# Optimization experiments

Measured on AMD Instinct MI355X. Metric: run time of the kernel, lower is better.

## Reference

```python
import jax, jax.numpy as jnp
import numpy as np

N, DEG, F, H, OUT = 50000, 16, 128, 128, 64


def _lstm_aggr(neigh, w_ih, w_hh, b_ih, b_hh):
    # neigh: [N, D, F] fixed-degree neighbor features; run LSTM over D steps,
    # return final hidden state [N, H] (PyG SAGEConv 'lstm' aggregation).
    n, d, f = neigh.shape
    h_dim = w_hh.shape[1]

    def step(carry, xt):
        h, c = carry
        gates = xt @ w_ih.T + b_ih + h @ w_hh.T + b_hh  # [N, 4H]
        i, fg, g, o = jnp.split(gates, 4, axis=-1)      # torch gate order i,f,g,o
        i = jax.nn.sigmoid(i)
        fg = jax.nn.sigmoid(fg)
        g = jnp.tanh(g)
        o = jax.nn.sigmoid(o)
        c = fg * c + i * g
        h = o * jnp.tanh(c)
        return (h, c), None

    h0 = jnp.zeros((n, h_dim), neigh.dtype)
    (h, _), _ = jax.lax.scan(step, (h0, h0), jnp.swapaxes(neigh, 0, 1))
    return h


def _sage_lstm(x, src, w_ih, w_hh, b_ih, b_hh, wl, bl, wr):
    # SAGEConv: out = lin_l(lstm_aggr(x[neighbors])) + lin_r(x)
    neigh = x[src]                                   # [N, D, F] gather
    aggr = _lstm_aggr(neigh, w_ih, w_hh, b_ih, b_hh)  # [N, H]
    return aggr @ wl.T + bl + x @ wr.T


def setup_inputs() -> dict:
    key = jax.random.key(0)
    ks = jax.random.split(key, 16)
    x = jax.random.normal(ks[0], (N, F), dtype=jnp.float32)
    # fixed-degree graph: dst = arange(N) each repeated DEG times (sorted, as
    # PyG lstm aggregation requires), src random -> edge_index [2, N*DEG]
    src = jax.random.randint(ks[1], (N * DEG,), 0, N, dtype=jnp.int64)
    dst = jnp.repeat(jnp.arange(N, dtype=jnp.int64), DEG)
    edge_index = jnp.stack([src, dst])
    s = 1.0 / np.sqrt(H)
    def u(k, shape):
        return jax.random.uniform(k, shape, jnp.float32, -s, s)
    params = {
        # layer 1 (input F -> hidden H)
        "w_ih1": u(ks[2], (4 * H, F)), "w_hh1": u(ks[3], (4 * H, H)),
        "b_ih1": u(ks[4], (4 * H,)), "b_hh1": u(ks[5], (4 * H,)),
        "lin_l1_w": u(ks[6], (H, H)), "lin_l1_b": u(ks[6], (H,)),
        "lin_r1_w": u(ks[7], (H, F)),
        # layer 2 (H -> H)
        "w_ih2": u(ks[8], (4 * H, H)), "w_hh2": u(ks[9], (4 * H, H)),
        "b_ih2": u(ks[10], (4 * H,)), "b_hh2": u(ks[11], (4 * H,)),
        "lin_l2_w": u(ks[12], (H, H)), "lin_l2_b": u(ks[12], (H,)),
        "lin_r2_w": u(ks[13], (H, H)),
        # output head
        "lin_w": u(ks[14], (OUT, H)), "lin_b": u(ks[15], (OUT,)),
    }
    return {"x": x, "edge_index": edge_index, **params}


def reference(x, edge_index,
              w_ih1, w_hh1, b_ih1, b_hh1, lin_l1_w, lin_l1_b, lin_r1_w,
              w_ih2, w_hh2, b_ih2, b_hh2, lin_l2_w, lin_l2_b, lin_r2_w,
              lin_w, lin_b):
    n = x.shape[0]
    deg = edge_index.shape[1] // n
    src = edge_index[0].reshape(n, deg)  # fixed-degree neighbor matrix
    h = _sage_lstm(x, src, w_ih1, w_hh1, b_ih1, b_hh1, lin_l1_w, lin_l1_b, lin_r1_w)
    h = jax.nn.relu(h)
    h = _sage_lstm(h, src, w_ih2, w_hh2, b_ih2, b_hh2, lin_l2_w, lin_l2_b, lin_r2_w)
    h = jax.nn.relu(h)
    return h @ lin_w.T + lin_b
```

## Files before the change

kernel.cpp:

```cpp
#include <hip/hip_runtime.h>
#include <stdint.h>

#define NN 50000
#define DEG 16
#define MT 32
#define NBLK ((NN + MT - 1) / MT)
#define LOG2E 1.4426950408889634f

typedef short bf16x8 __attribute__((ext_vector_type(8)));
typedef float f32x4 __attribute__((ext_vector_type(4)));
typedef unsigned short u16;
typedef unsigned int u32;

static __device__ __forceinline__ u16 f2bf(float f) {
  union { float f; u32 u; } v; v.f = f;
  u32 u = v.u + 0x7FFFu + ((v.u >> 16) & 1u);
  return (u16)(u >> 16);
}
static __device__ __forceinline__ u32 cvtpk(float lo, float hi) {
  u32 r;
  asm("v_cvt_pk_bf16_f32 %0, %1, %2" : "=v"(r) : "v"(lo), "v"(hi));
  return r;
}
static __device__ __forceinline__ float rcp_(float x) {
  return __builtin_amdgcn_rcpf(x);
}
static __device__ __forceinline__ float ex2_(float x) {
  return __builtin_amdgcn_exp2f(x);
}
static __device__ __forceinline__ void gload_lds16(const void* g, void* l) {
  __builtin_amdgcn_global_load_lds(
      (const __attribute__((address_space(1))) void*)g,
      (__attribute__((address_space(3))) void*)l, 16, 0, 0);
}

__global__ void k_prep(const float* __restrict__ x, u16* __restrict__ xb,
                       const float* __restrict__ wih1, const float* __restrict__ whh1, u16* __restrict__ wpk1,
                       const float* __restrict__ wih2, const float* __restrict__ whh2, u16* __restrict__ wpk2,
                       const float* __restrict__ lr1, const float* __restrict__ ll1, u16* __restrict__ epk1,
                       const float* __restrict__ lr2, const float* __restrict__ ll2, u16* __restrict__ epk2,
                       const float* __restrict__ linw, u16* __restrict__ hpk,
                       const float* __restrict__ bi1, const float* __restrict__ bh1, float* __restrict__ bs1,
                       const float* __restrict__ bi2, const float* __restrict__ bh2, float* __restrict__ bs2) {
  int b = blockIdx.x;
  if (b < 128) {
    const float* wih = (b < 64) ? wih1 : wih2;
    const float* whh = (b < 64) ? whh1 : whh2;
    u16* wpk = (b < 64) ? wpk1 : wpk2;
    int t = (b & 63) * 256 + threadIdx.x;
    int lane = t & 63, kt = (t >> 6) & 7, g = (t >> 9) & 3, w = (t >> 11) & 7;
    int col = g * 128 + w * 16 + (lane & 15);
    int k0 = kt * 32 + (lane >> 4) * 8;
    float sc = (g == 2) ? 2.f * LOG2E : LOG2E;
#pragma unroll
    for (int j = 0; j < 8; ++j) {
      int k = k0 + j;
      float v = (k < 128) ? wih[col * 128 + k] : whh[col * 128 + k - 128];
      wpk[t * 8 + j] = f2bf(sc * v);
    }
  } else if (b < 160) {
    const float* lrw = (b < 144) ? lr1 : lr2;
    const float* llw = (b < 144) ? ll1 : ll2;
    u16* epk = (b < 144) ? epk1 : epk2;
    int t = ((b - 128) & 15) * 256 + threadIdx.x;
    int lane = t & 63, kt = (t >> 6) & 7, w = (t >> 9) & 7;
    int col = w * 16 + (lane & 15);
    int k0 = kt * 32 + (lane >> 4) * 8;
#pragma unroll
    for (int j = 0; j < 8; ++j) {
      int k = k0 + j;
      epk[t * 8 + j] = f2bf(k < 128 ? lrw[col * 128 + k] : llw[col * 128 + k - 128]);
    }
  } else if (b < 164) {
    int t = (b - 160) * 256 + threadIdx.x;
    int lane = t & 63, kt = (t >> 6) & 3, w = (t >> 8) & 3;
    int col = w * 16 + (lane & 15);
    int k0 = kt * 32 + (lane >> 4) * 8;
#pragma unroll
    for (int j = 0; j < 8; ++j) hpk[t * 8 + j] = f2bf(linw[col * 128 + k0 + j]);
  } else if (b < 168) {
    int t = (b - 164) * 256 + threadIdx.x;
    if (t < 1024) {
      int i = t & 511;
      float sc = ((i >> 7) == 2) ? 2.f * LOG2E : LOG2E;
      if (t < 512) bs1[i] = sc * (bi1[i] + bh1[i]);
      else bs2[i] = sc * (bi2[i] + bh2[i]);
    }
  } else {
    int i = (b - 168) * 256 + threadIdx.x;
    int stride = (gridDim.x - 168) * 256;
    for (; i < NN * 128 / 4; i += stride) {
      float4 v = ((const float4*)x)[i];
      ushort4 o;
      o.x = f2bf(v.x); o.y = f2bf(v.y); o.z = f2bf(v.z); o.w = f2bf(v.w);
      ((ushort4*)xb)[i] = o;
    }
  }
}


#define GATHER(DCODE, PDST)                                                   \
  do {                                                                        \
    int idx_;                                                                 \
    if ((DCODE) < DEG) idx_ = IDX[grow * DEG + (DCODE)];                      \
    else idx_ = (node0 + grow < NN) ? node0 + grow : NN - 1;                  \
    const char* gsw_ = (const char*)(xin + (size_t)idx_ * 128) +              \
                       ((lr * 16) ^ ((grow & 15) << 4));                      \
    gload_lds16(gsw_, (PDST) + (w * 4) * 128);                                \
  } while (0)

#define CBAR(N)                                                               \
  do {                                                                        \
    asm volatile("s_waitcnt vmcnt(" #N ") lgkmcnt(0)" ::: "memory");          \
    __builtin_amdgcn_s_barrier();                                             \
    __builtin_amdgcn_sched_barrier(0);                                        \
  } while (0)

template <int L2>
__global__ __launch_bounds__(512, 2) void k_layer(
    const u16* __restrict__ xin, const int* __restrict__ src,
    const u16* __restrict__ wpk, const float* __restrict__ bsum,
    const u16* __restrict__ epk, const float* __restrict__ linlb,
    u16* __restrict__ hout, const u16* __restrict__ hpk,
    const float* __restrict__ linb, float* __restrict__ dout) {
  __shared__ __align__(16) u16 AX[3][MT * 128];
  __shared__ __align__(16) u16 AH[2][MT * 128];
  __shared__ int IDX[MT * DEG];

  const int tid = threadIdx.x;
  const int w = tid >> 6, l = tid & 63;
  const int lr = l & 15, lh = l >> 4;
  const int node0 = blockIdx.x * MT;
  const int grow = w * 4 + lh;

  bf16x8 wreg[4][8];
#pragma unroll
  for (int g = 0; g < 4; ++g)
#pragma unroll
    for (int kt = 0; kt < 8; ++kt)
      wreg[g][kt] = *(const bf16x8*)(wpk + (size_t)(((w * 4 + g) * 8 + kt) * 64 + l) * 8);

  IDX[tid] = (node0 + (tid >> 4) < NN) ? src[node0 * DEG + tid] : 0;

  float gb[4];
#pragma unroll
  for (int g = 0; g < 4; ++g) gb[g] = bsum[g * 128 + w * 16 + lr];
  float eb = linlb[w * 16 + lr];
  __syncthreads();

  GATHER(0, AX[0]);
  GATHER(1, AX[1]);

  f32x4 c[2];
  c[0] = (f32x4){0.f, 0.f, 0.f, 0.f};
  c[1] = (f32x4){0.f, 0.f, 0.f, 0.f};
  CBAR(1);

  u16 *pA = AX[0], *pB = AX[1], *pC = AX[2];

#pragma unroll 1
  for (int step = 0; step < DEG; ++step) {
    const int cb = step & 1, nb = cb ^ 1;

    if (step < DEG - 1) GATHER(step + 2, pC);

    f32x4 acc[2][4];
#pragma unroll
    for (int mt = 0; mt < 2; ++mt)
#pragma unroll
      for (int g = 0; g < 4; ++g)
        acc[mt][g] = (f32x4){gb[g], gb[g], gb[g], gb[g]};

    __builtin_amdgcn_s_setprio(1);
#pragma unroll
    for (int kt = 0; kt < 4; ++kt) {
      bf16x8 af[2];
#pragma unroll
      for (int mt = 0; mt < 2; ++mt) {
        int row = mt * 16 + lr;
        af[mt] = *(const bf16x8*)((const char*)pA + row * 256 +
                                  ((kt * 64 + lh * 16) ^ ((row & 15) << 4)));
      }
#pragma unroll
      for (int g = 0; g < 4; ++g)
#pragma unroll
        for (int mt = 0; mt < 2; ++mt)
          acc[mt][g] = __builtin_amdgcn_mfma_f32_16x16x32_bf16(af[mt], wreg[g][kt], acc[mt][g], 0, 0, 0);
    }

    if (step) {
#pragma unroll
      for (int kt = 0; kt < 4; ++kt) {
        bf16x8 af[2];
#pragma unroll
        for (int mt = 0; mt < 2; ++mt) {
          int row = mt * 16 + lr;
          af[mt] = *(const bf16x8*)((const char*)AH[cb] + row * 256 +
                                    ((kt * 64 + lh * 16) ^ ((row & 15) << 4)));
        }
#pragma unroll
        for (int g = 0; g < 4; ++g)
#pragma unroll
          for (int mt = 0; mt < 2; ++mt)
            acc[mt][g] = __builtin_amdgcn_mfma_f32_16x16x32_bf16(af[mt], wreg[g][4 + kt], acc[mt][g], 0, 0, 0);
      }
    }
    __builtin_amdgcn_s_setprio(0);

#pragma unroll
    for (int mt = 0; mt < 2; ++mt) {
      float hv[4];
#pragma unroll
      for (int r = 0; r < 4; ++r) {
        float iv = rcp_(1.f + ex2_(-acc[mt][0][r]));
        float fv = rcp_(1.f + ex2_(-acc[mt][1][r]));
        float gv = 1.f - 2.f * rcp_(1.f + ex2_(acc[mt][2][r]));
        float ov = rcp_(1.f + ex2_(-acc[mt][3][r]));
        float cv = fv * c[mt][r] + iv * gv;
        c[mt][r] = cv;
        float th = 1.f - 2.f * rcp_(1.f + ex2_(2.f * LOG2E * cv));
        hv[r] = ov * th;
      }
      u32 pk01 = cvtpk(hv[0], hv[1]);
      u32 pk23 = cvtpk(hv[2], hv[3]);
      const int jj = 2 * (w * 16 + lr);
#pragma unroll
      for (int r = 0; r < 4; ++r) {
        int row = mt * 16 + lh * 4 + r;
        u16 hb16 = (r == 0) ? (u16)pk01 : (r == 1) ? (u16)(pk01 >> 16)
                   : (r == 2) ? (u16)pk23 : (u16)(pk23 >> 16);
        *(u16*)((char*)AH[nb] + row * 256 + (jj ^ ((row & 15) << 4))) = hb16;
      }
    }

    if (step < DEG - 1) CBAR(1);
    else CBAR(0);

    u16* t_ = pA; pA = pB; pB = t_;
    t_ = pB; pB = pC; pC = t_;
  }

  f32x4 eacc[2];
  eacc[0] = (f32x4){eb, eb, eb, eb};
  eacc[1] = (f32x4){eb, eb, eb, eb};
#pragma unroll
  for (int kt = 0; kt < 8; ++kt) {
    const u16* srcb = (kt < 4) ? pA : AH[0];
    int kb = (kt & 3) * 64 + lh * 16;
    bf16x8 af[2];
#pragma unroll
    for (int mt = 0; mt < 2; ++mt) {
      int row = mt * 16 + lr;
      af[mt] = *(const bf16x8*)((const char*)srcb + row * 256 +
                                (kb ^ ((row & 15) << 4)));
    }
    bf16x8 bf = *(const bf16x8*)(epk + (size_t)((w * 8 + kt) * 64 + l) * 8);
#pragma unroll
    for (int mt = 0; mt < 2; ++mt)
      eacc[mt] = __builtin_amdgcn_mfma_f32_16x16x32_bf16(af[mt], bf, eacc[mt], 0, 0, 0);
  }

  if constexpr (!L2) {
#pragma unroll
    for (int mt = 0; mt < 2; ++mt) {
      u32 pk01 = cvtpk(fmaxf(eacc[mt][0], 0.f), fmaxf(eacc[mt][1], 0.f));
      u32 pk23 = cvtpk(fmaxf(eacc[mt][2], 0.f), fmaxf(eacc[mt][3], 0.f));
#pragma unroll
      for (int r = 0; r < 4; ++r) {
        int node = node0 + mt * 16 + lh * 4 + r;
        if (node < NN) {
          u16 hb16 = (r == 0) ? (u16)pk01 : (r == 1) ? (u16)(pk01 >> 16)
                     : (r == 2) ? (u16)pk23 : (u16)(pk23 >> 16);
          hout[(size_t)node * 128 + w * 16 + lr] = hb16;
        }
      }
    }
  } else {
#pragma unroll
    for (int mt = 0; mt < 2; ++mt) {
      u32 pk01 = cvtpk(fmaxf(eacc[mt][0], 0.f), fmaxf(eacc[mt][1], 0.f));
      u32 pk23 = cvtpk(fmaxf(eacc[mt][2], 0.f), fmaxf(eacc[mt][3], 0.f));
      const int jj = 2 * (w * 16 + lr);
#pragma unroll
      for (int r = 0; r < 4; ++r) {
        int row = mt * 16 + lh * 4 + r;
        u16 hb16 = (r == 0) ? (u16)pk01 : (r == 1) ? (u16)(pk01 >> 16)
                   : (r == 2) ? (u16)pk23 : (u16)(pk23 >> 16);
        *(u16*)((char*)AH[1] + row * 256 + (jj ^ ((row & 15) << 4))) = hb16;
      }
    }
    __syncthreads();
    if (w < 4) {
      float hb = linb[w * 16 + lr];
      f32x4 hacc[2];
      hacc[0] = (f32x4){hb, hb, hb, hb};
      hacc[1] = (f32x4){hb, hb, hb, hb};
#pragma unroll
      for (int kt = 0; kt < 4; ++kt) {
        bf16x8 af[2];
#pragma unroll
        for (int mt = 0; mt < 2; ++mt) {
          int row = mt * 16 + lr;
          af[mt] = *(const bf16x8*)((const char*)AH[1] + row * 256 +
                                    ((kt * 64 + lh * 16) ^ ((row & 15) << 4)));
        }
        bf16x8 bf = *(const bf16x8*)(hpk + (size_t)((w * 4 + kt) * 64 + l) * 8);
#pragma unroll
        for (int mt = 0; mt < 2; ++mt)
          hacc[mt] = __builtin_amdgcn_mfma_f32_16x16x32_bf16(af[mt], bf, hacc[mt], 0, 0, 0);
      }
#pragma unroll
      for (int mt = 0; mt < 2; ++mt)
#pragma unroll
        for (int r = 0; r < 4; ++r) {
          int node = node0 + mt * 16 + lh * 4 + r;
          if (node < NN) dout[(size_t)node * 64 + w * 16 + lr] = hacc[mt][r];
        }
    }
  }
}

extern "C" void kernel_launch(void* const* d_in, const int* in_sizes, int n_in,
                              void* d_out, int out_size, void* d_ws, size_t ws_size,
                              hipStream_t stream) {
  const float* x    = (const float*)d_in[0];
  const int*   edge = (const int*)d_in[1];
  const float* wih1 = (const float*)d_in[2];
  const float* whh1 = (const float*)d_in[3];
  const float* bih1 = (const float*)d_in[4];
  const float* bhh1 = (const float*)d_in[5];
  const float* ll1w = (const float*)d_in[6];
  const float* ll1b = (const float*)d_in[7];
  const float* lr1w = (const float*)d_in[8];
  const float* wih2 = (const float*)d_in[9];
  const float* whh2 = (const float*)d_in[10];
  const float* bih2 = (const float*)d_in[11];
  const float* bhh2 = (const float*)d_in[12];
  const float* ll2w = (const float*)d_in[13];
  const float* ll2b = (const float*)d_in[14];
  const float* lr2w = (const float*)d_in[15];
  const float* linw = (const float*)d_in[16];
  const float* linb = (const float*)d_in[17];

  char* ws = (char*)d_ws;
  u16* xb    = (u16*)(ws);
  u16* h1b   = (u16*)(ws + 12800000);
  u16* wpk1  = (u16*)(ws + 25600000);
  u16* wpk2  = (u16*)(ws + 25862144);
  u16* epk1  = (u16*)(ws + 26124288);
  u16* epk2  = (u16*)(ws + 26189824);
  u16* hpk   = (u16*)(ws + 26255360);
  float* bs1 = (float*)(ws + 26271744);
  float* bs2 = (float*)(ws + 26273792);

  k_prep<<<1000, 256, 0, stream>>>(x, xb,
                                   wih1, whh1, wpk1, wih2, whh2, wpk2,
                                   lr1w, ll1w, epk1, lr2w, ll2w, epk2,
                                   linw, hpk,
                                   bih1, bhh1, bs1, bih2, bhh2, bs2);
  k_layer<0><<<NBLK, 512, 0, stream>>>(xb, edge, wpk1, bs1, epk1, ll1b,
                                       h1b, nullptr, nullptr, nullptr);
  k_layer<1><<<NBLK, 512, 0, stream>>>(h1b, edge, wpk2, bs2, epk2, ll2b,
                                       nullptr, hpk, linb, (float*)d_out);
}
```

Measured before the change: 497.9 us.

## Software-pipeline the LSTM input projection one step ahead with a 4-deep gather ring

The input-to-gate MFMA work (x_t · W_ih) for the next time step now runs before the end-of-step barrier, right after the elementwise gate update. After the barrier, only the recurrent h · W_hh part sits on the critical path of each step. To keep data ready, the neighbor-gather ring grows from 3 to 4 LDS buffers and prefetches three steps ahead. The cost is more LDS per block and accumulator registers held live across the barrier, which could add register pressure under the 512-thread, 2-block launch bounds.

```diff
diff --git a/kernel.cpp b/kernel.cpp
--- a/kernel.cpp
+++ b/kernel.cpp
@@ -116,6 +116,26 @@
     __builtin_amdgcn_sched_barrier(0);                                        \
   } while (0)
 
+#define XPART(P)                                                              \
+  do {                                                                        \
+    _Pragma("unroll") for (int mt = 0; mt < 2; ++mt)                          \
+        _Pragma("unroll") for (int g = 0; g < 4; ++g)                         \
+            acc[mt][g] = (f32x4){gb[g], gb[g], gb[g], gb[g]};                 \
+    __builtin_amdgcn_s_setprio(1);                                            \
+    _Pragma("unroll") for (int kt = 0; kt < 4; ++kt) {                        \
+      bf16x8 af[2];                                                           \
+      _Pragma("unroll") for (int mt = 0; mt < 2; ++mt) {                      \
+        int row = mt * 16 + lr;                                               \
+        af[mt] = *(const bf16x8*)((const char*)(P) + row * 256 +              \
+                                  ((kt * 64 + lh * 16) ^ ((row & 15) << 4))); \
+      }                                                                       \
+      _Pragma("unroll") for (int g = 0; g < 4; ++g)                           \
+          _Pragma("unroll") for (int mt = 0; mt < 2; ++mt)                    \
+              acc[mt][g] = __builtin_amdgcn_mfma_f32_16x16x32_bf16(af[mt], wreg[g][kt], acc[mt][g], 0, 0, 0); \
+    }                                                                         \
+    __builtin_amdgcn_s_setprio(0);                                            \
+  } while (0)
+
 template <int L2>
 __global__ __launch_bounds__(512, 2) void k_layer(
     const u16* __restrict__ xin, const int* __restrict__ src,
@@ -123,7 +143,7 @@
     const u16* __restrict__ epk, const float* __restrict__ linlb,
     u16* __restrict__ hout, const u16* __restrict__ hpk,
     const float* __restrict__ linb, float* __restrict__ dout) {
-  __shared__ __align__(16) u16 AX[3][MT * 128];
+  __shared__ __align__(16) u16 AX[4][MT * 128];
   __shared__ __align__(16) u16 AH[2][MT * 128];
   __shared__ int IDX[MT * DEG];
 
@@ -150,45 +170,27 @@
 
   GATHER(0, AX[0]);
   GATHER(1, AX[1]);
+  GATHER(2, AX[2]);
 
   f32x4 c[2];
   c[0] = (f32x4){0.f, 0.f, 0.f, 0.f};
   c[1] = (f32x4){0.f, 0.f, 0.f, 0.f};
+
+  u16 *p0 = AX[0], *p1 = AX[1], *p2 = AX[2], *p3 = AX[3];
+
   CBAR(1);
 
-  u16 *pA = AX[0], *pB = AX[1], *pC = AX[2];
+  f32x4 acc[2][4];
+  XPART(p0);
 
 #pragma unroll 1
   for (int step = 0; step < DEG; ++step) {
     const int cb = step & 1, nb = cb ^ 1;
 
-    if (step < DEG - 1) GATHER(step + 2, pC);
-
-    f32x4 acc[2][4];
-#pragma unroll
-    for (int mt = 0; mt < 2; ++mt)
-#pragma unroll
-      for (int g = 0; g < 4; ++g)
-        acc[mt][g] = (f32x4){gb[g], gb[g], gb[g], gb[g]};
-
-    __builtin_amdgcn_s_setprio(1);
-#pragma unroll
-    for (int kt = 0; kt < 4; ++kt) {
-      bf16x8 af[2];
-#pragma unroll
-      for (int mt = 0; mt < 2; ++mt) {
-        int row = mt * 16 + lr;
-        af[mt] = *(const bf16x8*)((const char*)pA + row * 256 +
-                                  ((kt * 64 + lh * 16) ^ ((row & 15) << 4)));
-      }
-#pragma unroll
-      for (int g = 0; g < 4; ++g)
-#pragma unroll
-        for (int mt = 0; mt < 2; ++mt)
-          acc[mt][g] = __builtin_amdgcn_mfma_f32_16x16x32_bf16(af[mt], wreg[g][kt], acc[mt][g], 0, 0, 0);
-    }
+    if (step < DEG - 2) GATHER(step + 3, p3);
 
     if (step) {
+      __builtin_amdgcn_s_setprio(1);
 #pragma unroll
       for (int kt = 0; kt < 4; ++kt) {
         bf16x8 af[2];
@@ -204,8 +206,8 @@
           for (int mt = 0; mt < 2; ++mt)
             acc[mt][g] = __builtin_amdgcn_mfma_f32_16x16x32_bf16(af[mt], wreg[g][4 + kt], acc[mt][g], 0, 0, 0);
       }
-    }
-    __builtin_amdgcn_s_setprio(0);
+      __builtin_amdgcn_s_setprio(0);
+    }
 
 #pragma unroll
     for (int mt = 0; mt < 2; ++mt) {
@@ -233,11 +235,12 @@
       }
     }
 
+    if (step < DEG - 1) XPART(p1);
+
     if (step < DEG - 1) CBAR(1);
     else CBAR(0);
 
-    u16* t_ = pA; pA = pB; pB = t_;
-    t_ = pB; pB = pC; pC = t_;
+    u16* t_ = p0; p0 = p1; p1 = p2; p2 = p3; p3 = t_;
   }
 
   f32x4 eacc[2];
@@ -245,7 +248,7 @@
   eacc[1] = (f32x4){eb, eb, eb, eb};
 #pragma unroll
   for (int kt = 0; kt < 8; ++kt) {
-    const u16* srcb = (kt < 4) ? pA : AH[0];
+    const u16* srcb = (kt < 4) ? p0 : AH[0];
     int kb = (kt & 3) * 64 + lh * 16;
     bf16x8 af[2];
 #pragma unroll
```

Measured after the change: 538.6 us. +8.2%, slower.
